# Kernel optimization log

Hardware: AMD Instinct MI355X
Metric: run time of the kernel (lower is better)

Reference implementation:

```python
import jax, jax.numpy as jnp
import numpy as np


def _cdist(a, b, p):
    # a: [B, N, D], b: [B, M, D] -> [B, N, M] pairwise Lp distance
    diff = jnp.abs(a[:, :, None, :] - b[:, None, :, :])  # [B, N, M, D]
    if p == 1:
        return jnp.sum(diff, axis=-1)
    return jnp.sum(diff ** p, axis=-1) ** (1.0 / p)


def setup_inputs() -> dict:
    key = jax.random.key(0)
    k1, k2, k3 = jax.random.split(key, 3)
    B, P, D = 32, 2048, 2
    pred = jax.random.normal(k1, (B, P, D), dtype=jnp.float32)
    gt = jax.random.normal(k2, (B, P, D), dtype=jnp.float32)
    gt_valid = jax.random.normal(k3, (B, P, D), dtype=jnp.float32)
    return {"pred": pred, "gt": gt, "gt_valid": gt_valid, "loss_type": 1}


def reference(pred, gt, gt_valid, loss_type):
    # matrix = cdist(pred, gt): [B, Np, Ng]; torch.min(dim=1) reduces over Np
    m1 = _cdist(pred, gt, loss_type)
    pred2gt_min = jnp.min(m1, axis=1)  # [B, Ng]
    # matrix = cdist(gt_valid, pred): [B, Ngv, Np]; min over dim=1 (Ngv)
    m2 = _cdist(gt_valid, pred, loss_type)
    gt2pred_min = jnp.min(m2, axis=1)  # [B, Np]
    return jnp.mean(jnp.stack([jnp.mean(pred2gt_min), jnp.mean(gt2pred_min)]))
```

## Files before the change

kernel.cpp:

```cpp
#include <hip/hip_runtime.h>


#define BB 32
#define NN 2048
#define TPB 256
#define TGTS 64
#define WAVES 4
#define CH (NN / WAVES)
#define NTILES (NN / TGTS)
#define NBLK (2 * BB * NTILES)

__global__ __launch_bounds__(TPB) void chamfer_l1_part(
    const float* __restrict__ pred,
    const float* __restrict__ gt,
    const float* __restrict__ gt_valid,
    float* __restrict__ bsum)
{
    const int bid  = blockIdx.x;
    const int dir  = bid >> 10;
    const int rem  = bid & 1023;
    const int b    = rem >> 5;
    const int tile = rem & (NTILES - 1);
    const int lane = threadIdx.x & 63;
    const int wid  = __builtin_amdgcn_readfirstlane(threadIdx.x >> 6);

    const int j = tile * TGTS + lane;

    const float* __restrict__ tgt = (dir == 0 ? gt   : pred)     + (size_t)b * NN * 2;
    const float* __restrict__ src = (dir == 0 ? pred : gt_valid) + (size_t)b * NN * 2
                                    + (size_t)wid * CH * 2;

    const float px = tgt[2 * j];
    const float py = tgt[2 * j + 1];

    float m0 = 1e30f, m1 = 1e30f, m2 = 1e30f, m3 = 1e30f;
    #pragma unroll 2
    for (int s = 0; s < CH; s += 8) {
        float4 qa = *reinterpret_cast<const float4*>(src + 2 * s + 0);
        float4 qb = *reinterpret_cast<const float4*>(src + 2 * s + 4);
        float4 qc = *reinterpret_cast<const float4*>(src + 2 * s + 8);
        float4 qd = *reinterpret_cast<const float4*>(src + 2 * s + 12);
        float d0 = fabsf(px - qa.x) + fabsf(py - qa.y);
        float d1 = fabsf(px - qa.z) + fabsf(py - qa.w);
        float d2 = fabsf(px - qb.x) + fabsf(py - qb.y);
        float d3 = fabsf(px - qb.z) + fabsf(py - qb.w);
        float d4 = fabsf(px - qc.x) + fabsf(py - qc.y);
        float d5 = fabsf(px - qc.z) + fabsf(py - qc.w);
        float d6 = fabsf(px - qd.x) + fabsf(py - qd.y);
        float d7 = fabsf(px - qd.z) + fabsf(py - qd.w);
        m0 = fminf(m0, fminf(d0, d1));
        m1 = fminf(m1, fminf(d2, d3));
        m2 = fminf(m2, fminf(d4, d5));
        m3 = fminf(m3, fminf(d6, d7));
    }
    float m = fminf(fminf(m0, m1), fminf(m2, m3));

    __shared__ float part[WAVES][TGTS];
    part[wid][lane] = m;
    __syncthreads();
    if (wid == 0) {
        float mm = fminf(fminf(part[0][lane], part[1][lane]),
                         fminf(part[2][lane], part[3][lane]));
        for (int off = 32; off > 0; off >>= 1)
            mm += __shfl_down(mm, off, 64);
        if (lane == 0) bsum[bid] = mm;
    }
}

__global__ __launch_bounds__(TPB) void chamfer_l1_reduce(
    const float* __restrict__ bsum,
    float* __restrict__ out)
{
    const int t = threadIdx.x;
    float4 v0 = reinterpret_cast<const float4*>(bsum)[2 * t];
    float4 v1 = reinterpret_cast<const float4*>(bsum)[2 * t + 1];
    float s = (v0.x + v0.y) + (v0.z + v0.w) + (v1.x + v1.y) + (v1.z + v1.w);
    for (int off = 32; off > 0; off >>= 1)
        s += __shfl_down(s, off, 64);
    __shared__ float w[TPB / 64];
    if ((t & 63) == 0) w[t >> 6] = s;
    __syncthreads();
    if (t == 0)
        out[0] = (w[0] + w[1] + w[2] + w[3]) * (1.0f / (2.0f * BB * NN));
}

extern "C" void kernel_launch(void* const* d_in, const int* in_sizes, int n_in,
                              void* d_out, int out_size, void* d_ws, size_t ws_size,
                              hipStream_t stream) {
    const float* pred     = (const float*)d_in[0];
    const float* gt       = (const float*)d_in[1];
    const float* gt_valid = (const float*)d_in[2];
    float* out  = (float*)d_out;
    float* bsum = (float*)d_ws;

    chamfer_l1_part<<<NBLK, TPB, 0, stream>>>(pred, gt, gt_valid, bsum);
    chamfer_l1_reduce<<<1, TPB, 0, stream>>>(bsum, out);
}
```

Measured before the change: 83.98 us.

## Compute two targets per lane with packed f32 subtract and wider blocks

Measured after the change: 83.94 us. Within noise of the previous version (-0.0%).

```diff
diff --git a/kernel.cpp b/kernel.cpp
--- a/kernel.cpp
+++ b/kernel.cpp
@@ -1,14 +1,22 @@
 #include <hip/hip_runtime.h>
 
 
+typedef float v2f __attribute__((ext_vector_type(2)));
+
 #define BB 32
 #define NN 2048
-#define TPB 256
-#define TGTS 64
-#define WAVES 4
+#define TPB 512
+#define WAVES 8
+#define TGT 128
 #define CH (NN / WAVES)
-#define NTILES (NN / TGTS)
+#define NTILES (NN / TGT)
 #define NBLK (2 * BB * NTILES)
+
+__device__ __forceinline__ v2f pk_diff(v2f q_uniform, v2f negp) {
+    v2f d;
+    asm("v_pk_add_f32 %0, %1, %2" : "=v"(d) : "s"(q_uniform), "v"(negp));
+    return d;
+}
 
 __global__ __launch_bounds__(TPB) void chamfer_l1_part(
     const float* __restrict__ pred,
@@ -17,67 +25,90 @@
     float* __restrict__ bsum)
 {
     const int bid  = blockIdx.x;
-    const int dir  = bid >> 10;
-    const int rem  = bid & 1023;
-    const int b    = rem >> 5;
+    const int dir  = bid >> 9;
+    const int rem  = bid & 511;
+    const int b    = rem >> 4;
     const int tile = rem & (NTILES - 1);
     const int lane = threadIdx.x & 63;
     const int wid  = __builtin_amdgcn_readfirstlane(threadIdx.x >> 6);
-
-    const int j = tile * TGTS + lane;
 
     const float* __restrict__ tgt = (dir == 0 ? gt   : pred)     + (size_t)b * NN * 2;
     const float* __restrict__ src = (dir == 0 ? pred : gt_valid) + (size_t)b * NN * 2
                                     + (size_t)wid * CH * 2;
 
-    const float px = tgt[2 * j];
-    const float py = tgt[2 * j + 1];
+    const int j0 = tile * TGT + lane;
+    const int j1 = j0 + 64;
 
-    float m0 = 1e30f, m1 = 1e30f, m2 = 1e30f, m3 = 1e30f;
+    v2f npA, npB;
+    {
+        float2 pA = reinterpret_cast<const float2*>(tgt)[j0];
+        float2 pB = reinterpret_cast<const float2*>(tgt)[j1];
+        npA = (v2f){-pA.x, -pA.y};
+        npB = (v2f){-pB.x, -pB.y};
+    }
+
+    float a0 = 1e30f, a1 = 1e30f, b0 = 1e30f, b1 = 1e30f;
+    const float4* __restrict__ srcv = reinterpret_cast<const float4*>(src);
     #pragma unroll 2
-    for (int s = 0; s < CH; s += 8) {
-        float4 qa = *reinterpret_cast<const float4*>(src + 2 * s + 0);
-        float4 qb = *reinterpret_cast<const float4*>(src + 2 * s + 4);
-        float4 qc = *reinterpret_cast<const float4*>(src + 2 * s + 8);
-        float4 qd = *reinterpret_cast<const float4*>(src + 2 * s + 12);
-        float d0 = fabsf(px - qa.x) + fabsf(py - qa.y);
-        float d1 = fabsf(px - qa.z) + fabsf(py - qa.w);
-        float d2 = fabsf(px - qb.x) + fabsf(py - qb.y);
-        float d3 = fabsf(px - qb.z) + fabsf(py - qb.w);
-        float d4 = fabsf(px - qc.x) + fabsf(py - qc.y);
-        float d5 = fabsf(px - qc.z) + fabsf(py - qc.w);
-        float d6 = fabsf(px - qd.x) + fabsf(py - qd.y);
-        float d7 = fabsf(px - qd.z) + fabsf(py - qd.w);
-        m0 = fminf(m0, fminf(d0, d1));
-        m1 = fminf(m1, fminf(d2, d3));
-        m2 = fminf(m2, fminf(d4, d5));
-        m3 = fminf(m3, fminf(d6, d7));
+    for (int s = 0; s < CH / 2; s += 2) {
+        float4 qa = srcv[s];
+        float4 qb = srcv[s + 1];
+        v2f q0 = (v2f){qa.x, qa.y};
+        v2f q1 = (v2f){qa.z, qa.w};
+        v2f q2 = (v2f){qb.x, qb.y};
+        v2f q3 = (v2f){qb.z, qb.w};
+
+        v2f dA0 = pk_diff(q0, npA), dA1 = pk_diff(q1, npA);
+        v2f dA2 = pk_diff(q2, npA), dA3 = pk_diff(q3, npA);
+        v2f dB0 = pk_diff(q0, npB), dB1 = pk_diff(q1, npB);
+        v2f dB2 = pk_diff(q2, npB), dB3 = pk_diff(q3, npB);
+
+        float sA0 = fabsf(dA0.x) + fabsf(dA0.y);
+        float sA1 = fabsf(dA1.x) + fabsf(dA1.y);
+        float sA2 = fabsf(dA2.x) + fabsf(dA2.y);
+        float sA3 = fabsf(dA3.x) + fabsf(dA3.y);
+        float sB0 = fabsf(dB0.x) + fabsf(dB0.y);
+        float sB1 = fabsf(dB1.x) + fabsf(dB1.y);
+        float sB2 = fabsf(dB2.x) + fabsf(dB2.y);
+        float sB3 = fabsf(dB3.x) + fabsf(dB3.y);
+
+        a0 = fminf(a0, fminf(sA0, sA1));
+        a1 = fminf(a1, fminf(sA2, sA3));
+        b0 = fminf(b0, fminf(sB0, sB1));
+        b1 = fminf(b1, fminf(sB2, sB3));
     }
-    float m = fminf(fminf(m0, m1), fminf(m2, m3));
+    const float mA = fminf(a0, a1);
+    const float mB = fminf(b0, b1);
 
-    __shared__ float part[WAVES][TGTS];
-    part[wid][lane] = m;
+    __shared__ float part[WAVES][TGT];
+    part[wid][lane]      = mA;
+    part[wid][64 + lane] = mB;
     __syncthreads();
-    if (wid == 0) {
-        float mm = fminf(fminf(part[0][lane], part[1][lane]),
-                         fminf(part[2][lane], part[3][lane]));
+
+    __shared__ float wpart[2];
+    if (threadIdx.x < 128) {
+        const int t = threadIdx.x;
+        float mm = part[0][t];
+        #pragma unroll
+        for (int w = 1; w < WAVES; ++w) mm = fminf(mm, part[w][t]);
         for (int off = 32; off > 0; off >>= 1)
             mm += __shfl_down(mm, off, 64);
-        if (lane == 0) bsum[bid] = mm;
+        if ((t & 63) == 0) wpart[t >> 6] = mm;
     }
+    __syncthreads();
+    if (threadIdx.x == 0) bsum[bid] = wpart[0] + wpart[1];
 }
 
-__global__ __launch_bounds__(TPB) void chamfer_l1_reduce(
+__global__ __launch_bounds__(256) void chamfer_l1_reduce(
     const float* __restrict__ bsum,
     float* __restrict__ out)
 {
     const int t = threadIdx.x;
-    float4 v0 = reinterpret_cast<const float4*>(bsum)[2 * t];
-    float4 v1 = reinterpret_cast<const float4*>(bsum)[2 * t + 1];
-    float s = (v0.x + v0.y) + (v0.z + v0.w) + (v1.x + v1.y) + (v1.z + v1.w);
+    float4 v = reinterpret_cast<const float4*>(bsum)[t];
+    float s = (v.x + v.y) + (v.z + v.w);
     for (int off = 32; off > 0; off >>= 1)
         s += __shfl_down(s, off, 64);
-    __shared__ float w[TPB / 64];
+    __shared__ float w[4];
     if ((t & 63) == 0) w[t >> 6] = s;
     __syncthreads();
     if (t == 0)
@@ -94,5 +125,5 @@
     float* bsum = (float*)d_ws;
 
     chamfer_l1_part<<<NBLK, TPB, 0, stream>>>(pred, gt, gt_valid, bsum);
-    chamfer_l1_reduce<<<1, TPB, 0, stream>>>(bsum, out);
+    chamfer_l1_reduce<<<1, 256, 0, stream>>>(bsum, out);
 }
```
